# Performance work log

Measured on AMD Instinct MI355X. Metric: run time of the kernel, lower is better.

Reference implementation:

```python
import jax, jax.numpy as jnp
import numpy as np

B, SQ, SK, H, NH = 2, 2048, 2048, 1024, 16
HD = H // NH  # 64 per-head dim


def gelu(x):
    # GPT-2 tanh-approx gelu
    return 0.5 * x * (1.0 + jnp.tanh(np.sqrt(2.0 / np.pi) * (x + 0.044715 * x ** 3)))


def setup_inputs() -> dict:
    key = jax.random.key(0)
    ks = jax.random.split(key, 9)
    std = 0.02
    return {
        "attender_seq": jax.random.normal(ks[0], (B, SQ, H), jnp.float32),
        "attendee_seq": jax.random.normal(ks[1], (B, SK, H), jnp.float32),
        "attendee_mask": jax.random.randint(ks[2], (B, SK), 0, 2, jnp.int32),
        "c_attn_w": std * jax.random.normal(ks[3], (H, 3 * H), jnp.float32),
        "c_attn_b": jnp.zeros((3 * H,), jnp.float32),
        "c_proj_w": std * jax.random.normal(ks[4], (H, H), jnp.float32),
        "c_proj_b": jnp.zeros((H,), jnp.float32),
        "mlp_w": std * jax.random.normal(ks[5], (2 * H, H), jnp.float32),
        "mlp_b": jnp.zeros((H,), jnp.float32),
    }


def reference(attender_seq, attendee_seq, attendee_mask,
              c_attn_w, c_attn_b, c_proj_w, c_proj_b, mlp_w, mlp_b):
    # Conv1D == affine: x @ W + b
    qkv_q = attender_seq @ c_attn_w + c_attn_b   # [B,SQ,3H]
    qkv_k = attendee_seq @ c_attn_w + c_attn_b   # [B,SK,3H]
    q = qkv_q[..., :H]
    k = qkv_k[..., H:2 * H]
    v = qkv_k[..., 2 * H:]

    q = q.reshape(B, SQ, NH, HD)
    k = k.reshape(B, SK, NH, HD)
    v = v.reshape(B, SK, NH, HD)

    scores = jnp.einsum('bqhd,bkhd->bhqk', q, k)  # no 1/sqrt(d): scale=False
    # multiplicative (not additive) mask applied post-score, pre-softmax
    scores = scores * attendee_mask.astype(scores.dtype)[:, None, None, :]
    probs = jax.nn.softmax(scores, axis=-1)
    attn = jnp.einsum('bhqk,bkhd->bqhd', probs, v).reshape(B, SQ, H)
    attn = attn @ c_proj_w + c_proj_b            # [B,SQ,H]

    cat = jnp.concatenate([attender_seq, attn], axis=2)  # [B,SQ,2H]
    out = gelu(cat @ mlp_w + mlp_b)              # [B,SQ,H] (dropout = eval identity)
    return out
```

## Files before the change

### kernel.cpp

```cpp
#include <hip/hip_runtime.h>
#include <hip/hip_bf16.h>
#include <math.h>

#define H_ 1024
#define NH_ 16
#define HD_ 64
#define B_ 2
#define SQ_ 2048
#define SK_ 2048

using bf16x8 = __attribute__((ext_vector_type(8))) short;
using f32x4  = __attribute__((ext_vector_type(4))) float;
using f32x16 = __attribute__((ext_vector_type(16))) float;

static __device__ __forceinline__ unsigned short f2bf(float f) {
  union { float f; unsigned u; } v; v.f = f;
  unsigned r = v.u + 0x7fffu + ((v.u >> 16) & 1u);
  return (unsigned short)(r >> 16);
}

static __device__ __forceinline__ unsigned cvtpk(float a, float b) {
  unsigned r;
  asm("v_cvt_pk_bf16_f32 %0, %1, %2" : "=v"(r) : "v"(a), "v"(b));
  return r;
}

static __device__ __forceinline__ void gl2lds16(const void* g, void* l) {
  __builtin_amdgcn_global_load_lds(
      (const __attribute__((address_space(1))) unsigned int*)g,
      (__attribute__((address_space(3))) unsigned int*)l, 16, 0, 0);
}

static __device__ __forceinline__ int sidx(int row, int cbyte) {
  return row * 64 + (((cbyte) ^ ((row & 7) << 4)) >> 1);
}

__global__ __launch_bounds__(256) void conv_act(
    const float* __restrict__ att, const float* __restrict__ ate,
    unsigned short* __restrict__ cat, unsigned short* __restrict__ aet) {
  const long NV = (long)4096 * 1024 / 8;
  for (long i = blockIdx.x * 256L + threadIdx.x; i < 2 * NV;
       i += (long)gridDim.x * 256) {
    const float* s;
    unsigned short* d;
    if (i < NV) {
      long e = i * 8;
      int r = (int)(e >> 10), c = (int)(e & 1023);
      s = att + e;
      d = cat + (long)r * 2048 + c;
    } else {
      long e = (i - NV) * 8;
      s = ate + e;
      d = aet + e;
    }
    unsigned short tmp[8];
#pragma unroll
    for (int j = 0; j < 8; ++j) tmp[j] = f2bf(s[j]);
    *(uint4*)d = *(uint4*)tmp;
  }
}

__global__ __launch_bounds__(256) void convT3(
    const float* __restrict__ w_at, const float* __restrict__ w_pr,
    const float* __restrict__ w_ml, unsigned short* __restrict__ o_at,
    unsigned short* __restrict__ o_pr, unsigned short* __restrict__ o_ml) {
  __shared__ __align__(16) unsigned short Ls[64][68];
  int bx = blockIdx.x;
  const float* in;
  unsigned short* out;
  int R, C;
  if (bx < 768) {
    in = w_at; out = o_at; R = 1024; C = 3072;
  } else if (bx < 1024) {
    in = w_pr; out = o_pr; R = 1024; C = 1024; bx -= 768;
  } else {
    in = w_ml; out = o_ml; R = 2048; C = 1024; bx -= 1024;
  }
  int nct = C >> 6;
  int tr = bx / nct, tc = bx % nct;
  int r0 = tr * 64, c0 = tc * 64;
  int rr = threadIdx.x >> 4;
  int cc = (threadIdx.x & 15) * 4;
#pragma unroll
  for (int i = 0; i < 4; ++i) {
    int r = rr + 16 * i;
    float4 v = *(const float4*)&in[(long)(r0 + r) * C + c0 + cc];
    unsigned short t[4] = {f2bf(v.x), f2bf(v.y), f2bf(v.z), f2bf(v.w)};
    *(unsigned long long*)&Ls[r][cc] = *(unsigned long long*)t;
  }
  __syncthreads();
  int oc = threadIdx.x >> 2;
  int orr = (threadIdx.x & 3) * 16;
  unsigned short t[16];
#pragma unroll
  for (int j = 0; j < 16; ++j) t[j] = Ls[orr + j][oc];
  *(uint4*)&out[(long)(c0 + oc) * R + r0 + orr] = *(uint4*)&t[0];
  *(uint4*)&out[(long)(c0 + oc) * R + r0 + orr + 8] = *(uint4*)&t[8];
}

template <int NF, int MODE>
__global__ __launch_bounds__(256) void gemm_bt(
    const unsigned short* __restrict__ A, int lda,
    const unsigned short* __restrict__ Bw, int ldb,
    const float* __restrict__ bias, const int* __restrict__ msk, float oscale,
    void* __restrict__ out0, void* __restrict__ out1, int ldo, int K) {
  __shared__ __align__(16) unsigned short Al[2][128 * 64];
  __shared__ __align__(16) unsigned short Bl[2][NF * 32 * 64];
  const int tid = threadIdx.x;
  const int l = tid & 63, w = tid >> 6;
  const int wr = w >> 1, wc = w & 1;
  const int lq = l & 15, lh = l >> 4;
  const int m0 = blockIdx.y * 128, n0 = blockIdx.x * (NF * 32);

  const int swcol = (((tid & 7) ^ ((tid >> 3) & 7)) << 3);
  const int rbase = w * 8 + (l >> 3);
  const unsigned short* gA = A + (long)(m0 + rbase) * lda + swcol;
  const unsigned short* gB = Bw + (long)(n0 + rbase) * ldb + swcol;

  f32x4 acc[4][NF];
#pragma unroll
  for (int a = 0; a < 4; ++a)
#pragma unroll
    for (int b = 0; b < NF; ++b) acc[a][b] = (f32x4){0.f, 0.f, 0.f, 0.f};

  auto stage = [&](int k0, int buf) {
#pragma unroll
    for (int i = 0; i < 4; ++i)
      gl2lds16(gA + (long)(i * 32) * lda + k0, &Al[buf][i * 2048 + w * 512]);
#pragma unroll
    for (int i = 0; i < NF; ++i)
      gl2lds16(gB + (long)(i * 32) * ldb + k0, &Bl[buf][i * 2048 + w * 512]);
  };

  const int NT = K >> 6;
  stage(0, 0);
  __syncthreads();
  int cur = 0;
  for (int t = 0; t < NT; ++t) {
    if (t + 1 < NT) stage((t + 1) << 6, cur ^ 1);
    bf16x8 af[4][2], bfr[NF][2];
#pragma unroll
    for (int a = 0; a < 4; ++a) {
      int row = wr * 64 + a * 16 + lq;
#pragma unroll
      for (int kk = 0; kk < 2; ++kk)
        af[a][kk] = *(const bf16x8*)&Al[cur][sidx(row, kk * 64 + lh * 16)];
    }
#pragma unroll
    for (int b = 0; b < NF; ++b) {
      int row = wc * (NF * 16) + b * 16 + lq;
#pragma unroll
      for (int kk = 0; kk < 2; ++kk)
        bfr[b][kk] = *(const bf16x8*)&Bl[cur][sidx(row, kk * 64 + lh * 16)];
    }
#pragma unroll
    for (int kk = 0; kk < 2; ++kk)
#pragma unroll
      for (int a = 0; a < 4; ++a)
#pragma unroll
        for (int b = 0; b < NF; ++b)
          acc[a][b] = __builtin_amdgcn_mfma_f32_16x16x32_bf16(
              af[a][kk], bfr[b][kk], acc[a][b], 0, 0, 0);
    __syncthreads();
    cur ^= 1;
  }

#pragma unroll
  for (int a = 0; a < 4; ++a) {
#pragma unroll
    for (int bb = 0; bb < NF; ++bb) {
      int col = n0 + wc * (NF * 16) + bb * 16 + lq;
      float bv = bias[col];
      int row0 = m0 + wr * 64 + a * 16 + lh * 4;
      if (MODE == 0) {
        unsigned short* O = (unsigned short*)out0;
#pragma unroll
        for (int r = 0; r < 4; ++r)
          O[(long)(row0 + r) * ldo + col] = f2bf((acc[a][bb][r] + bv) * oscale);
      } else if (MODE == 1) {
        float* O = (float*)out0;
#pragma unroll
        for (int r = 0; r < 4; ++r) {
          float v = acc[a][bb][r] + bv;
          float y = 0.7978845608028654f * (v + 0.044715f * v * v * v);
          O[(long)(row0 + r) * ldo + col] =
              v * __builtin_amdgcn_rcpf(1.f + __expf(-2.f * y));
        }
      } else {
        if (col < H_) {
          unsigned short* O = (unsigned short*)out0;
#pragma unroll
          for (int r = 0; r < 4; ++r) {
            float mk = (float)msk[row0 + r];
            O[(long)(row0 + r) * ldo + col] = f2bf((acc[a][bb][r] + bv) * mk);
          }
        } else {
          int vcol = col - H_, hh = vcol >> 6, dd = vcol & 63;
          int bi = row0 >> 11, k = row0 & 2047;
          unsigned short t[4];
#pragma unroll
          for (int r = 0; r < 4; ++r) t[r] = f2bf(acc[a][bb][r] + bv);
          *(unsigned long long*)((unsigned short*)out1 +
                                 (((long)(bi * NH_ + hh) * HD_ + dd) << 11) + k) =
              *(unsigned long long*)t;
        }
      }
    }
  }
}

__global__ __launch_bounds__(256) void flash_attn(
    const unsigned short* __restrict__ Qb,
    const unsigned short* __restrict__ Kb,
    const unsigned short* __restrict__ Vtg,
    unsigned short* __restrict__ Ob) {
  __shared__ __align__(16) unsigned short Kl[2][64 * 64];
  __shared__ __align__(16) unsigned short Vl[2][64 * 64];
  __shared__ __align__(16) float Lr[4][32];
  const int tid = threadIdx.x;
  const int l = tid & 63, w = tid >> 6;
  const int lo = l & 31, hi = l >> 5;
  const int id = blockIdx.x;
  const int xcd = id & 7, sub = id >> 3;
  const int pair = xcd * 4 + (sub >> 4);
  const int qb = sub & 15;
  const int b = pair >> 4, h = pair & 15;
  const int brow = b * SQ_ + qb * 128 + w * 32;

  bf16x8 qf[4];
  {
    const unsigned short* qp = Qb + (long)(brow + lo) * H_ + h * HD_ + hi * 8;
#pragma unroll
    for (int d = 0; d < 4; ++d) qf[d] = *(const bf16x8*)(qp + d * 16);
  }

  const int srow = w * 8 + (l >> 3);
  const int swc = ((l & 7) ^ ((l >> 3) & 7)) << 3;
  const unsigned short* Kg = Kb + ((long)b * SK_ + srow) * H_ + h * HD_ + swc;
  const unsigned short* Vg = Vtg + ((long)(b * NH_ + h) * HD_ + srow) * SK_ + swc;

  auto stage = [&](int kt, int buf) {
    const unsigned short* ks = Kg + (long)kt * 64 * H_;
    const unsigned short* vs = Vg + kt * 64;
    char* kd = (char*)&Kl[buf][0] + w * 1024;
    char* vd = (char*)&Vl[buf][0] + w * 1024;
    gl2lds16(ks, kd);
    gl2lds16(ks + (long)32 * H_, kd + 4096);
    gl2lds16(vs, vd);
    gl2lds16(vs + (long)32 * SK_, vd + 4096);
  };

  f32x16 accO[2];
#pragma unroll
  for (int i = 0; i < 2; ++i)
#pragma unroll
    for (int r = 0; r < 16; ++r) accO[i][r] = 0.f;
  float l_run = 0.f;

  stage(0, 0);
  __syncthreads();
  int cur = 0;
  const int NT = SK_ / 64;
  for (int kt = 0; kt < NT; ++kt) {
    if (kt + 1 < NT) stage(kt + 1, cur ^ 1);
    const unsigned short* Kc = &Kl[cur][0];
    const unsigned short* Vc = &Vl[cur][0];

    f32x16 s0, s1;
#pragma unroll
    for (int r = 0; r < 16; ++r) { s0[r] = 0.f; s1[r] = 0.f; }
    __builtin_amdgcn_s_setprio(1);
#pragma unroll
    for (int ds = 0; ds < 4; ++ds) {
      bf16x8 ka0 = *(const bf16x8*)&Kc[sidx(lo, ds * 32 + hi * 16)];
      bf16x8 ka1 = *(const bf16x8*)&Kc[sidx(32 + lo, ds * 32 + hi * 16)];
      s0 = __builtin_amdgcn_mfma_f32_32x32x16_bf16(ka0, qf[ds], s0, 0, 0, 0);
      s1 = __builtin_amdgcn_mfma_f32_32x32x16_bf16(ka1, qf[ds], s1, 0, 0, 0);
    }
    __builtin_amdgcn_s_setprio(0);

    bf16x8 pa[4];
    float ps = 0.f;
#pragma unroll
    for (int kh = 0; kh < 2; ++kh) {
      const f32x16& s = kh ? s1 : s0;
      float p[16];
#pragma unroll
      for (int r = 0; r < 16; ++r) { p[r] = exp2f(s[r]); ps += p[r]; }
#pragma unroll
      for (int g = 0; g < 2; ++g) {
        unsigned X0 = cvtpk(p[g * 8 + 0], p[g * 8 + 1]);
        unsigned X1 = cvtpk(p[g * 8 + 2], p[g * 8 + 3]);
        unsigned Y0 = cvtpk(p[g * 8 + 4], p[g * 8 + 5]);
        unsigned Y1 = cvtpk(p[g * 8 + 6], p[g * 8 + 7]);
        asm("v_permlane32_swap_b32 %0, %1" : "+v"(X0), "+v"(Y0));
        asm("v_permlane32_swap_b32 %0, %1" : "+v"(X1), "+v"(Y1));
        union { unsigned u[4]; bf16x8 v; } cc;
        cc.u[0] = X0; cc.u[1] = X1; cc.u[2] = Y0; cc.u[3] = Y1;
        pa[kh * 2 + g] = cc.v;
      }
    }
    l_run += ps;

    __builtin_amdgcn_s_setprio(1);
#pragma unroll
    for (int dh = 0; dh < 2; ++dh)
#pragma unroll
      for (int ks = 0; ks < 4; ++ks) {
        bf16x8 vb = *(const bf16x8*)&Vc[sidx(dh * 32 + lo, ks * 32 + hi * 16)];
        accO[dh] = __builtin_amdgcn_mfma_f32_32x32x16_bf16(pa[ks], vb, accO[dh], 0, 0, 0);
      }
    __builtin_amdgcn_s_setprio(0);
    __syncthreads();
    cur ^= 1;
  }

  l_run += __shfl_xor(l_run, 32);
  if (l < 32) Lr[w][lo] = __builtin_amdgcn_rcpf(l_run);
  f32x4 rsq[4];
#pragma unroll
  for (int rq = 0; rq < 4; ++rq)
    rsq[rq] = *(const f32x4*)&Lr[w][4 * hi + 8 * rq];

#pragma unroll
  for (int dh = 0; dh < 2; ++dh) {
#pragma unroll
    for (int r = 0; r < 16; ++r) {
      int qm = 4 * hi + (r & 3) + 8 * (r >> 2);
      float v = accO[dh][r] * rsq[r >> 2][r & 3];
      Ob[(long)(brow + qm) * H_ + h * HD_ + dh * 32 + lo] = f2bf(v);
    }
  }
}

extern "C" void kernel_launch(void* const* d_in, const int* in_sizes, int n_in,
                              void* d_out, int out_size, void* d_ws, size_t ws_size,
                              hipStream_t stream) {
  (void)in_sizes; (void)n_in; (void)out_size; (void)ws_size;
  const float* attender = (const float*)d_in[0];
  const float* attendee = (const float*)d_in[1];
  const int*   mask     = (const int*)d_in[2];
  const float* c_attn_w = (const float*)d_in[3];
  const float* c_attn_b = (const float*)d_in[4];
  const float* c_proj_w = (const float*)d_in[5];
  const float* c_proj_b = (const float*)d_in[6];
  const float* mlp_w    = (const float*)d_in[7];
  const float* mlp_b    = (const float*)d_in[8];
  float* out = (float*)d_out;

  char* ws = (char*)d_ws;
  size_t off = 0;
  auto alloc = [&](size_t bytes) {
    void* p = ws + off;
    off += (bytes + 255) & ~(size_t)255;
    return p;
  };
  unsigned short* cat   = (unsigned short*)alloc((size_t)4096 * 2048 * 2);
  unsigned short* aet   = (unsigned short*)alloc((size_t)4096 * 1024 * 2);
  unsigned short* w_atT = (unsigned short*)alloc((size_t)3072 * 1024 * 2);
  unsigned short* w_prT = (unsigned short*)alloc((size_t)1024 * 1024 * 2);
  unsigned short* w_mlT = (unsigned short*)alloc((size_t)1024 * 2048 * 2);
  unsigned short* Qb    = (unsigned short*)alloc((size_t)4096 * 1024 * 2);
  unsigned short* Kbuf  = (unsigned short*)alloc((size_t)4096 * 1024 * 2);
  unsigned short* Vtg   = (unsigned short*)alloc((size_t)B_ * NH_ * HD_ * SK_ * 2);
  unsigned short* attnb = (unsigned short*)alloc((size_t)4096 * 1024 * 2);

  const float LOG2E = 1.4426950408889634f;

  conv_act<<<2048, 256, 0, stream>>>(attender, attendee, cat, aet);
  convT3<<<1536, 256, 0, stream>>>(c_attn_w, c_proj_w, mlp_w, w_atT, w_prT, w_mlT);

  gemm_bt<2, 0><<<dim3(16, 32), 256, 0, stream>>>(
      cat, 2048, w_atT, 1024, c_attn_b, nullptr, LOG2E, Qb, nullptr, 1024, 1024);
  gemm_bt<4, 2><<<dim3(16, 32), 256, 0, stream>>>(
      aet, 1024, w_atT + (size_t)1024 * 1024, 1024, c_attn_b + 1024, mask, 1.f,
      Kbuf, Vtg, 1024, 1024);
  flash_attn<<<512, 256, 0, stream>>>(Qb, Kbuf, Vtg, attnb);
  gemm_bt<2, 0><<<dim3(16, 32), 256, 0, stream>>>(
      attnb, 1024, w_prT, 1024, c_proj_b, nullptr, 1.f, cat + 1024, nullptr, 2048, 1024);
  gemm_bt<2, 1><<<dim3(16, 32), 256, 0, stream>>>(
      cat, 2048, w_mlT, 2048, mlp_b, nullptr, 1.f, out, nullptr, 1024, 2048);
}
```

Measured before the change: 173.3 us.

## Split flash attention over two key halves and combine partials in separate kernel

The attention kernel now splits the key sequence into two halves, doubling the grid to 1024 blocks. Each block writes an unnormalized fp32 partial output and row sum, and a new combine kernel adds the two halves, normalizes, and writes bf16. Since softmax here uses no running max, the partials combine by simple addition. The aim is better CU occupancy, at the cost of an extra launch and fp32 partial traffic. The score MFMA chain also starts from a zero register instead of zeroing accumulators each tile.

```diff
diff --git a/kernel.cpp b/kernel.cpp
--- a/kernel.cpp
+++ b/kernel.cpp
@@ -213,17 +213,17 @@
     const unsigned short* __restrict__ Qb,
     const unsigned short* __restrict__ Kb,
     const unsigned short* __restrict__ Vtg,
-    unsigned short* __restrict__ Ob) {
+    float* __restrict__ Op, float* __restrict__ Lp) {
   __shared__ __align__(16) unsigned short Kl[2][64 * 64];
   __shared__ __align__(16) unsigned short Vl[2][64 * 64];
-  __shared__ __align__(16) float Lr[4][32];
   const int tid = threadIdx.x;
   const int l = tid & 63, w = tid >> 6;
   const int lo = l & 31, hi = l >> 5;
   const int id = blockIdx.x;
   const int xcd = id & 7, sub = id >> 3;
-  const int pair = xcd * 4 + (sub >> 4);
-  const int qb = sub & 15;
+  const int pair = xcd * 4 + (sub >> 5);
+  const int rem = sub & 31;
+  const int qb = rem & 15, sp = rem >> 4;
   const int b = pair >> 4, h = pair & 15;
   const int brow = b * SQ_ + qb * 128 + w * 32;
 
@@ -250,30 +250,33 @@
     gl2lds16(vs + (long)32 * SK_, vd + 4096);
   };
 
-  f32x16 accO[2];
+  f32x16 zreg, accO[2];
+#pragma unroll
+  for (int r = 0; r < 16; ++r) zreg[r] = 0.f;
 #pragma unroll
   for (int i = 0; i < 2; ++i)
 #pragma unroll
     for (int r = 0; r < 16; ++r) accO[i][r] = 0.f;
   float l_run = 0.f;
 
-  stage(0, 0);
+  const int kt0 = sp * 16, kt1 = kt0 + 16;
+  stage(kt0, 0);
   __syncthreads();
   int cur = 0;
-  const int NT = SK_ / 64;
-  for (int kt = 0; kt < NT; ++kt) {
-    if (kt + 1 < NT) stage(kt + 1, cur ^ 1);
+  for (int kt = kt0; kt < kt1; ++kt) {
+    if (kt + 1 < kt1) stage(kt + 1, cur ^ 1);
     const unsigned short* Kc = &Kl[cur][0];
     const unsigned short* Vc = &Vl[cur][0];
 
-    f32x16 s0, s1;
-#pragma unroll
-    for (int r = 0; r < 16; ++r) { s0[r] = 0.f; s1[r] = 0.f; }
     __builtin_amdgcn_s_setprio(1);
-#pragma unroll
-    for (int ds = 0; ds < 4; ++ds) {
-      bf16x8 ka0 = *(const bf16x8*)&Kc[sidx(lo, ds * 32 + hi * 16)];
-      bf16x8 ka1 = *(const bf16x8*)&Kc[sidx(32 + lo, ds * 32 + hi * 16)];
+    bf16x8 ka0 = *(const bf16x8*)&Kc[sidx(lo, hi * 16)];
+    bf16x8 ka1 = *(const bf16x8*)&Kc[sidx(32 + lo, hi * 16)];
+    f32x16 s0 = __builtin_amdgcn_mfma_f32_32x32x16_bf16(ka0, qf[0], zreg, 0, 0, 0);
+    f32x16 s1 = __builtin_amdgcn_mfma_f32_32x32x16_bf16(ka1, qf[0], zreg, 0, 0, 0);
+#pragma unroll
+    for (int ds = 1; ds < 4; ++ds) {
+      ka0 = *(const bf16x8*)&Kc[sidx(lo, ds * 32 + hi * 16)];
+      ka1 = *(const bf16x8*)&Kc[sidx(32 + lo, ds * 32 + hi * 16)];
       s0 = __builtin_amdgcn_mfma_f32_32x32x16_bf16(ka0, qf[ds], s0, 0, 0, 0);
       s1 = __builtin_amdgcn_mfma_f32_32x32x16_bf16(ka1, qf[ds], s1, 0, 0, 0);
     }
@@ -316,20 +319,38 @@
   }
 
   l_run += __shfl_xor(l_run, 32);
-  if (l < 32) Lr[w][lo] = __builtin_amdgcn_rcpf(l_run);
-  f32x4 rsq[4];
-#pragma unroll
-  for (int rq = 0; rq < 4; ++rq)
-    rsq[rq] = *(const f32x4*)&Lr[w][4 * hi + 8 * rq];
-
+  const long rrow = (long)pair * SQ_ + qb * 128 + w * 32;
+  if (l < 32) Lp[(long)sp * (32 * SQ_) + rrow + lo] = l_run;
+  float* Ow = Op + (long)sp * ((long)32 * SQ_ * HD_);
 #pragma unroll
   for (int dh = 0; dh < 2; ++dh) {
 #pragma unroll
     for (int r = 0; r < 16; ++r) {
       int qm = 4 * hi + (r & 3) + 8 * (r >> 2);
-      float v = accO[dh][r] * rsq[r >> 2][r & 3];
-      Ob[(long)(brow + qm) * H_ + h * HD_ + dh * 32 + lo] = f2bf(v);
-    }
+      Ow[(rrow + qm) * HD_ + dh * 32 + lo] = accO[dh][r];
+    }
+  }
+}
+
+__global__ __launch_bounds__(256) void combine_o(
+    const float* __restrict__ Op, const float* __restrict__ Lp,
+    unsigned short* __restrict__ attnb) {
+  const long SS = (long)32 * SQ_ * HD_;
+  const int SL = 32 * SQ_;
+  const long total = (long)SL * (HD_ / 4);
+  for (long i = blockIdx.x * 256L + threadIdx.x; i < total;
+       i += (long)gridDim.x * 256) {
+    int row = (int)(i >> 4);
+    int d0 = (int)(i & 15) * 4;
+    float4 o0 = *(const float4*)&Op[(long)row * HD_ + d0];
+    float4 o1 = *(const float4*)&Op[SS + (long)row * HD_ + d0];
+    float rl = __builtin_amdgcn_rcpf(Lp[row] + Lp[SL + row]);
+    int pair = row >> 11, q = row & 2047;
+    int b = pair >> 4, h = pair & 15;
+    unsigned short t[4] = {f2bf((o0.x + o1.x) * rl), f2bf((o0.y + o1.y) * rl),
+                           f2bf((o0.z + o1.z) * rl), f2bf((o0.w + o1.w) * rl)};
+    *(unsigned long long*)&attnb[(long)(b * SQ_ + q) * H_ + h * HD_ + d0] =
+        *(unsigned long long*)t;
   }
 }
 
@@ -364,6 +385,8 @@
   unsigned short* Kbuf  = (unsigned short*)alloc((size_t)4096 * 1024 * 2);
   unsigned short* Vtg   = (unsigned short*)alloc((size_t)B_ * NH_ * HD_ * SK_ * 2);
   unsigned short* attnb = (unsigned short*)alloc((size_t)4096 * 1024 * 2);
+  float* Opart = (float*)alloc((size_t)2 * 32 * SQ_ * HD_ * 4);
+  float* Lpart = (float*)alloc((size_t)2 * 32 * SQ_ * 4);
 
   const float LOG2E = 1.4426950408889634f;
 
@@ -375,7 +398,8 @@
   gemm_bt<4, 2><<<dim3(16, 32), 256, 0, stream>>>(
       aet, 1024, w_atT + (size_t)1024 * 1024, 1024, c_attn_b + 1024, mask, 1.f,
       Kbuf, Vtg, 1024, 1024);
-  flash_attn<<<512, 256, 0, stream>>>(Qb, Kbuf, Vtg, attnb);
+  flash_attn<<<1024, 256, 0, stream>>>(Qb, Kbuf, Vtg, Opart, Lpart);
+  combine_o<<<2048, 256, 0, stream>>>(Opart, Lpart, attnb);
   gemm_bt<2, 0><<<dim3(16, 32), 256, 0, stream>>>(
       attnb, 1024, w_prT, 1024, c_proj_b, nullptr, 1.f, cat + 1024, nullptr, 2048, 1024);
   gemm_bt<2, 1><<<dim3(16, 32), 256, 0, stream>>>(
```

Result: slower. 186.1 us (+7.4%).
